# Performance work log

Measured on AMD Instinct MI355X. Metric: run time of the kernel, lower is better.

Reference implementation:

```python
import jax, jax.numpy as jnp
import numpy as np

B, E = 256, 512
C, K = 8192, 10          # n_class, n_center
LMD = 10.0
INV_GAMMA = 10.0         # 1 / gamma, gamma = 0.1
TAU = 0.2
MARGIN = 0.01


def setup_inputs() -> dict:
    key = jax.random.key(0)
    k1, k2, k3 = jax.random.split(key, 3)
    embeddings = jax.random.normal(k1, (B, E), dtype=jnp.float32)
    labels = jax.random.randint(k2, (B,), 0, C, dtype=jnp.int64)
    fc = jax.random.normal(k3, (C * K, E), dtype=jnp.float32)
    return {"embeddings": embeddings, "labels": labels, "fc": fc}


def reference(embeddings, labels, fc):
    # L2-normalize centers (rows of fc), like F.normalize(fc, p=2, dim=1)
    norm = jnp.sqrt(jnp.sum(fc * fc, axis=1, keepdims=True))
    w = fc / jnp.maximum(norm, 1e-12)

    # similarity to every center: [B, C, K]
    x = (embeddings @ w.T).reshape(B, C, K)
    prob = jax.nn.softmax(INV_GAMMA * x, axis=2)
    h = jnp.sum(prob * x, axis=2)  # [B, C] soft-pooled class similarity

    # subtract margin on ground-truth class, then cross-entropy
    rows = jnp.arange(B)
    margin_m = jnp.zeros_like(h).at[rows, labels].set(MARGIN)
    logits = LMD * (h - margin_m)
    logp = jax.nn.log_softmax(logits, axis=1)
    loss_cls = -jnp.mean(logp[rows, labels])

    # regularizer: batched per-class center gram, replaces python loop over C
    wc = w.reshape(C, K, E)
    sub = 1.0 - jnp.einsum('cke,cje->ckj', wc, wc)   # [C, K, K]
    sub = jnp.where(sub <= 0.0, 1e-10, sub)
    mask = jnp.triu(jnp.ones((K, K), dtype=bool), k=1)  # strict upper triangle
    safe = jnp.where(mask, 2.0 * sub, 1.0)
    reg = jnp.sum(jnp.where(mask, jnp.sqrt(safe), 0.0))
    reg = reg / (C * K * (K - 1.0))
    return loss_cls + TAU * reg
```

## Files before the change

### kernel.cpp

```cpp
#include <hip/hip_runtime.h>


typedef __bf16 bf16;
typedef bf16 bf16x8 __attribute__((ext_vector_type(8)));
typedef float f32x4 __attribute__((ext_vector_type(4)));

#define NCLASS 8192
#define KC 10
#define EDIM 512
#define BATCH 256

__device__ inline void load_lds16(const void* g, void* l) {
    __builtin_amdgcn_global_load_lds(
        (const __attribute__((address_space(1))) void*)g,
        (__attribute__((address_space(3))) void*)l, 16, 0, 0);
}

__global__ __launch_bounds__(256) void prep_kernel(
    const float* __restrict__ fc, bf16* __restrict__ w,
    float* __restrict__ gram_part)
{
    __shared__ float rows[KC * EDIM];
    __shared__ float s_invn[KC];
    __shared__ float s_wsum[4];
    const int c = blockIdx.x;
    const int t = threadIdx.x;
    const int wave = t >> 6, lane = t & 63;

    const float4* src = (const float4*)(fc + (size_t)c * (KC * EDIM));
    float4* rows4 = (float4*)rows;
    #pragma unroll
    for (int i = 0; i < 5; ++i) rows4[t + i * 256] = src[t + i * 256];
    __syncthreads();

    for (int r = wave; r < KC; r += 4) {
        float s = 0.f;
        #pragma unroll
        for (int j = 0; j < 8; ++j) {
            float v = rows[r * EDIM + lane + j * 64];
            s += v * v;
        }
        #pragma unroll
        for (int off = 32; off; off >>= 1) s += __shfl_xor(s, off);
        if (lane == 0) s_invn[r] = 1.0f / fmaxf(sqrtf(s), 1e-12f);
    }
    __syncthreads();

    bf16x8* dst = (bf16x8*)(w + (size_t)c * (KC * EDIM));
    #pragma unroll
    for (int p = 0; p < 3; ++p) {
        int j = t + p * 256;
        if (j < 640) {
            int r = j >> 6;
            float inv = s_invn[r];
            float4 a = *(const float4*)(rows + j * 8);
            float4 b = *(const float4*)(rows + j * 8 + 4);
            bf16x8 v;
            v[0] = (bf16)(a.x * inv); v[1] = (bf16)(a.y * inv);
            v[2] = (bf16)(a.z * inv); v[3] = (bf16)(a.w * inv);
            v[4] = (bf16)(b.x * inv); v[5] = (bf16)(b.y * inv);
            v[6] = (bf16)(b.z * inv); v[7] = (bf16)(b.w * inv);
            dst[j] = v;
        }
    }

    float part = 0.f;
    for (int p = wave; p < 45; p += 4) {
        int i = 0, pp = p;
        while (pp >= 9 - i) { pp -= 9 - i; ++i; }
        int j = i + 1 + pp;
        float s = 0.f;
        #pragma unroll
        for (int u = 0; u < 8; ++u)
            s += rows[i * EDIM + lane + u * 64] * rows[j * EDIM + lane + u * 64];
        #pragma unroll
        for (int off = 32; off; off >>= 1) s += __shfl_xor(s, off);
        if (lane == 0) {
            float sub = 1.0f - s * s_invn[i] * s_invn[j];
            if (sub <= 0.0f) sub = 1e-10f;
            part += sqrtf(2.0f * sub);
        }
    }
    if (lane == 0) s_wsum[wave] = part;
    __syncthreads();
    if (t == 0) gram_part[c] = s_wsum[0] + s_wsum[1] + s_wsum[2] + s_wsum[3];
}

__global__ __launch_bounds__(256) void conv_kernel(
    const float* __restrict__ e, bf16* __restrict__ out)
{
    int i = blockIdx.x * 256 + threadIdx.x;
    float4 a = ((const float4*)e)[i * 2];
    float4 b = ((const float4*)e)[i * 2 + 1];
    bf16x8 v;
    v[0] = (bf16)a.x; v[1] = (bf16)a.y; v[2] = (bf16)a.z; v[3] = (bf16)a.w;
    v[4] = (bf16)b.x; v[5] = (bf16)b.y; v[6] = (bf16)b.z; v[7] = (bf16)b.w;
    ((bf16x8*)out)[i] = v;
}

__global__ __launch_bounds__(512) void gemm_h_kernel(
    const bf16* __restrict__ W,
    const bf16* __restrict__ A,
    float* __restrict__ h)
{
    __shared__ bf16 Ws[80 * 32];
    __shared__ bf16 Es[256 * 32];
    const int tid = threadIdx.x;
    const int wave = tid >> 6, lane = tid & 63;

    f32x4 acc[5][2];
    #pragma unroll
    for (int mt = 0; mt < 5; ++mt)
        #pragma unroll
        for (int nt = 0; nt < 2; ++nt)
            acc[mt][nt] = (f32x4){0.f, 0.f, 0.f, 0.f};

    const size_t g0 = (size_t)blockIdx.x * 80;
    const int srow = lane >> 2;
    const int scol = (lane & 3) * 8;

    for (int kb = 0; kb < EDIM; kb += 32) {
        if (wave < 5)
            load_lds16(W + (g0 + (wave << 4) + srow) * EDIM + kb + scol,
                       Ws + ((wave << 4) * 32));
        #pragma unroll
        for (int p = 0; p < 2; ++p) {
            int row = p * 128 + wave * 16 + srow;
            load_lds16(A + row * EDIM + kb + scol,
                       Es + (p * 128 + wave * 16) * 32);
        }
        __syncthreads();

        const int q8 = (lane >> 4) * 8;
        const int fr = lane & 15;
        bf16x8 wf[5], ef[2];
        #pragma unroll
        for (int mt = 0; mt < 5; ++mt)
            wf[mt] = *(const bf16x8*)&Ws[(mt * 16 + fr) * 32 + q8];
        #pragma unroll
        for (int nt = 0; nt < 2; ++nt)
            ef[nt] = *(const bf16x8*)&Es[(wave * 32 + nt * 16 + fr) * 32 + q8];
        #pragma unroll
        for (int mt = 0; mt < 5; ++mt)
            #pragma unroll
            for (int nt = 0; nt < 2; ++nt)
                acc[mt][nt] = __builtin_amdgcn_mfma_f32_16x16x32_bf16(
                    wf[mt], ef[nt], acc[mt][nt], 0, 0, 0);
        __syncthreads();
    }

    const int col = lane & 15;
    const int quad = lane >> 4;
    const int cb = blockIdx.x * 8;
    #pragma unroll
    for (int nt = 0; nt < 2; ++nt) {
        int b = wave * 32 + nt * 16 + col;
        float hval[8];
        #pragma unroll
        for (int c = 0; c < 8; ++c) {
            float xm = -1e30f;
            #pragma unroll
            for (int mt = 0; mt < 5; ++mt) {
                if (10 * c + 10 > 16 * mt && 10 * c < 16 * mt + 16) {
                    #pragma unroll
                    for (int rg = 0; rg < 4; ++rg) {
                        int r = 16 * mt + 4 * quad + rg;
                        if (r >= 10 * c && r < 10 * c + 10)
                            xm = fmaxf(xm, acc[mt][nt][rg]);
                    }
                }
            }
            xm = fmaxf(xm, __shfl_xor(xm, 16));
            xm = fmaxf(xm, __shfl_xor(xm, 32));
            float s1 = 0.f, s2 = 0.f;
            #pragma unroll
            for (int mt = 0; mt < 5; ++mt) {
                if (10 * c + 10 > 16 * mt && 10 * c < 16 * mt + 16) {
                    #pragma unroll
                    for (int rg = 0; rg < 4; ++rg) {
                        int r = 16 * mt + 4 * quad + rg;
                        if (r >= 10 * c && r < 10 * c + 10) {
                            float x = acc[mt][nt][rg];
                            float e = __expf(10.0f * (x - xm));
                            s1 += e; s2 += e * x;
                        }
                    }
                }
            }
            s1 += __shfl_xor(s1, 16); s1 += __shfl_xor(s1, 32);
            s2 += __shfl_xor(s2, 16); s2 += __shfl_xor(s2, 32);
            hval[c] = s2 / s1;
        }
        if (quad == 0) {
            float4 v0 = {hval[0], hval[1], hval[2], hval[3]};
            float4 v1 = {hval[4], hval[5], hval[6], hval[7]};
            float4* dst = (float4*)&h[(size_t)b * NCLASS + cb];
            dst[0] = v0;
            dst[1] = v1;
        }
    }
}

__global__ __launch_bounds__(256) void ce_kernel(
    const float* __restrict__ h, const int* __restrict__ labels,
    float* __restrict__ ce_part)
{
    __shared__ float redm[4];
    __shared__ float reds[4];
    const int b = blockIdx.x, t = threadIdx.x;
    const int wave = t >> 6, lane = t & 63;
    const int lbl = labels[b];
    const float* hb = h + (size_t)b * NCLASS;

    float lg_cache[32];
    float mx = -1e30f;
    #pragma unroll
    for (int k = 0; k < 32; ++k) {
        int c = t + k * 256;
        float lg = 10.0f * hb[c];
        if (c == lbl) lg -= 0.1f;
        lg_cache[k] = lg;
        mx = fmaxf(mx, lg);
    }
    #pragma unroll
    for (int off = 32; off; off >>= 1) mx = fmaxf(mx, __shfl_xor(mx, off));
    if (lane == 0) redm[wave] = mx;
    __syncthreads();
    mx = fmaxf(fmaxf(redm[0], redm[1]), fmaxf(redm[2], redm[3]));

    float s = 0.f;
    #pragma unroll
    for (int k = 0; k < 32; ++k) s += __expf(lg_cache[k] - mx);
    #pragma unroll
    for (int off = 32; off; off >>= 1) s += __shfl_xor(s, off);
    if (lane == 0) reds[wave] = s;
    __syncthreads();
    if (t == 0) {
        s = reds[0] + reds[1] + reds[2] + reds[3];
        float logit_l = 10.0f * (hb[lbl] - 0.01f);
        ce_part[b] = mx + logf(s) - logit_l;
    }
}

__global__ __launch_bounds__(256) void final_kernel(
    const float* __restrict__ gram_part, const float* __restrict__ ce_part,
    float* __restrict__ out)
{
    __shared__ float red[4];
    const int t = threadIdx.x, wave = t >> 6, lane = t & 63;
    float g = 0.f;
    #pragma unroll
    for (int i = 0; i < 32; ++i) g += gram_part[t + i * 256];
    float val = ce_part[t] * (1.0f / 256.0f)
              + g * (0.2f / 737280.0f);
    #pragma unroll
    for (int off = 32; off; off >>= 1) val += __shfl_xor(val, off);
    if (lane == 0) red[wave] = val;
    __syncthreads();
    if (t == 0) out[0] = red[0] + red[1] + red[2] + red[3];
}

extern "C" void kernel_launch(void* const* d_in, const int* in_sizes, int n_in,
                              void* d_out, int out_size, void* d_ws, size_t ws_size,
                              hipStream_t stream) {
    const float* emb    = (const float*)d_in[0];
    const int*   labels = (const int*)d_in[1];
    const float* fc     = (const float*)d_in[2];
    float* out = (float*)d_out;

    char* ws = (char*)d_ws;
    bf16*  w         = (bf16*)ws;
    bf16*  embb      = (bf16*)(ws + 83886080);
    float* h         = (float*)(ws + 84148352);
    float* gram_part = (float*)(ws + 92536960);
    float* ce_part   = (float*)(ws + 92569728);

    prep_kernel<<<NCLASS, 256, 0, stream>>>(fc, w, gram_part);
    conv_kernel<<<64, 256, 0, stream>>>(emb, embb);
    gemm_h_kernel<<<81920 / 80, 512, 0, stream>>>(w, embb, h);
    ce_kernel<<<BATCH, 256, 0, stream>>>(h, labels, ce_part);
    final_kernel<<<1, 256, 0, stream>>>(gram_part, ce_part, out);
}
```

Measured before the change: 306.2 us.

## Fuse center normalization and gram regularizer into the GEMM kernel

Removes the separate prep kernel that wrote normalized bf16 centers to global memory. Each GEMM block now loads its 80 fp32 center rows straight into registers (one wave per class), computes row norms and the pairwise gram regularizer there, and writes the normalized bf16 rows into an XOR-swizzled LDS buffer holding the full K dimension. This drops the 80MB bf16 round trip to global memory and one kernel launch. In exchange each block needs about 96KB of LDS and holds many registers, which may limit occupancy, and the embedding tiles are still streamed per k-step.

```diff
diff --git a/kernel.cpp b/kernel.cpp
--- a/kernel.cpp
+++ b/kernel.cpp
@@ -14,76 +14,6 @@
     __builtin_amdgcn_global_load_lds(
         (const __attribute__((address_space(1))) void*)g,
         (__attribute__((address_space(3))) void*)l, 16, 0, 0);
-}
-
-__global__ __launch_bounds__(256) void prep_kernel(
-    const float* __restrict__ fc, bf16* __restrict__ w,
-    float* __restrict__ gram_part)
-{
-    __shared__ float rows[KC * EDIM];
-    __shared__ float s_invn[KC];
-    __shared__ float s_wsum[4];
-    const int c = blockIdx.x;
-    const int t = threadIdx.x;
-    const int wave = t >> 6, lane = t & 63;
-
-    const float4* src = (const float4*)(fc + (size_t)c * (KC * EDIM));
-    float4* rows4 = (float4*)rows;
-    #pragma unroll
-    for (int i = 0; i < 5; ++i) rows4[t + i * 256] = src[t + i * 256];
-    __syncthreads();
-
-    for (int r = wave; r < KC; r += 4) {
-        float s = 0.f;
-        #pragma unroll
-        for (int j = 0; j < 8; ++j) {
-            float v = rows[r * EDIM + lane + j * 64];
-            s += v * v;
-        }
-        #pragma unroll
-        for (int off = 32; off; off >>= 1) s += __shfl_xor(s, off);
-        if (lane == 0) s_invn[r] = 1.0f / fmaxf(sqrtf(s), 1e-12f);
-    }
-    __syncthreads();
-
-    bf16x8* dst = (bf16x8*)(w + (size_t)c * (KC * EDIM));
-    #pragma unroll
-    for (int p = 0; p < 3; ++p) {
-        int j = t + p * 256;
-        if (j < 640) {
-            int r = j >> 6;
-            float inv = s_invn[r];
-            float4 a = *(const float4*)(rows + j * 8);
-            float4 b = *(const float4*)(rows + j * 8 + 4);
-            bf16x8 v;
-            v[0] = (bf16)(a.x * inv); v[1] = (bf16)(a.y * inv);
-            v[2] = (bf16)(a.z * inv); v[3] = (bf16)(a.w * inv);
-            v[4] = (bf16)(b.x * inv); v[5] = (bf16)(b.y * inv);
-            v[6] = (bf16)(b.z * inv); v[7] = (bf16)(b.w * inv);
-            dst[j] = v;
-        }
-    }
-
-    float part = 0.f;
-    for (int p = wave; p < 45; p += 4) {
-        int i = 0, pp = p;
-        while (pp >= 9 - i) { pp -= 9 - i; ++i; }
-        int j = i + 1 + pp;
-        float s = 0.f;
-        #pragma unroll
-        for (int u = 0; u < 8; ++u)
-            s += rows[i * EDIM + lane + u * 64] * rows[j * EDIM + lane + u * 64];
-        #pragma unroll
-        for (int off = 32; off; off >>= 1) s += __shfl_xor(s, off);
-        if (lane == 0) {
-            float sub = 1.0f - s * s_invn[i] * s_invn[j];
-            if (sub <= 0.0f) sub = 1e-10f;
-            part += sqrtf(2.0f * sub);
-        }
-    }
-    if (lane == 0) s_wsum[wave] = part;
-    __syncthreads();
-    if (t == 0) gram_part[c] = s_wsum[0] + s_wsum[1] + s_wsum[2] + s_wsum[3];
 }
 
 __global__ __launch_bounds__(256) void conv_kernel(
@@ -98,16 +28,67 @@
     ((bf16x8*)out)[i] = v;
 }
 
-__global__ __launch_bounds__(512) void gemm_h_kernel(
-    const bf16* __restrict__ W,
+__global__ __launch_bounds__(512, 2) void fused_kernel(
+    const float* __restrict__ fc,
     const bf16* __restrict__ A,
-    float* __restrict__ h)
-{
-    __shared__ bf16 Ws[80 * 32];
+    float* __restrict__ h,
+    float* __restrict__ gram_part)
+{
+    __shared__ bf16 Wl[80 * EDIM];
     __shared__ bf16 Es[256 * 32];
     const int tid = threadIdx.x;
     const int wave = tid >> 6, lane = tid & 63;
 
+    const int c = blockIdx.x * 8 + wave;
+    float4 ra[KC][2];
+    #pragma unroll
+    for (int r = 0; r < KC; ++r) {
+        const float4* rp =
+            (const float4*)(fc + ((size_t)c * KC + r) * EDIM) + lane * 2;
+        ra[r][0] = rp[0];
+        ra[r][1] = rp[1];
+    }
+    float invn[KC];
+    #pragma unroll
+    for (int r = 0; r < KC; ++r) {
+        float4 a = ra[r][0], b = ra[r][1];
+        float s = a.x*a.x + a.y*a.y + a.z*a.z + a.w*a.w
+                + b.x*b.x + b.y*b.y + b.z*b.z + b.w*b.w;
+        #pragma unroll
+        for (int off = 32; off; off >>= 1) s += __shfl_xor(s, off);
+        invn[r] = 1.0f / fmaxf(sqrtf(s), 1e-12f);
+    }
+    float part = 0.f;
+    #pragma unroll
+    for (int i = 0; i < KC - 1; ++i) {
+        #pragma unroll
+        for (int j = i + 1; j < KC; ++j) {
+            float4 ai = ra[i][0], bi = ra[i][1];
+            float4 aj = ra[j][0], bj = ra[j][1];
+            float s = ai.x*aj.x + ai.y*aj.y + ai.z*aj.z + ai.w*aj.w
+                    + bi.x*bj.x + bi.y*bj.y + bi.z*bj.z + bi.w*bj.w;
+            #pragma unroll
+            for (int off = 32; off; off >>= 1) s += __shfl_xor(s, off);
+            float sub = 1.0f - s * invn[i] * invn[j];
+            if (sub <= 0.0f) sub = 1e-10f;
+            part += sqrtf(2.0f * sub);
+        }
+    }
+    if (lane == 0) gram_part[c] = part;
+
+    #pragma unroll
+    for (int r = 0; r < KC; ++r) {
+        int row = wave * KC + r;
+        float inv = invn[r];
+        float4 a = ra[r][0], b = ra[r][1];
+        bf16x8 v;
+        v[0] = (bf16)(a.x * inv); v[1] = (bf16)(a.y * inv);
+        v[2] = (bf16)(a.z * inv); v[3] = (bf16)(a.w * inv);
+        v[4] = (bf16)(b.x * inv); v[5] = (bf16)(b.y * inv);
+        v[6] = (bf16)(b.z * inv); v[7] = (bf16)(b.w * inv);
+        *(bf16x8*)&Wl[row * EDIM + ((lane ^ (row & 7)) << 3)] = v;
+    }
+
     f32x4 acc[5][2];
     #pragma unroll
     for (int mt = 0; mt < 5; ++mt)
@@ -115,14 +96,10 @@
         for (int nt = 0; nt < 2; ++nt)
             acc[mt][nt] = (f32x4){0.f, 0.f, 0.f, 0.f};
 
-    const size_t g0 = (size_t)blockIdx.x * 80;
     const int srow = lane >> 2;
     const int scol = (lane & 3) * 8;
 
     for (int kb = 0; kb < EDIM; kb += 32) {
-        if (wave < 5)
-            load_lds16(W + (g0 + (wave << 4) + srow) * EDIM + kb + scol,
-                       Ws + ((wave << 4) * 32));
         #pragma unroll
         for (int p = 0; p < 2; ++p) {
             int row = p * 128 + wave * 16 + srow;
@@ -135,8 +112,11 @@
         const int fr = lane & 15;
         bf16x8 wf[5], ef[2];
         #pragma unroll
-        for (int mt = 0; mt < 5; ++mt)
-            wf[mt] = *(const bf16x8*)&Ws[(mt * 16 + fr) * 32 + q8];
+        for (int mt = 0; mt < 5; ++mt) {
+            int row = mt * 16 + fr;
+            wf[mt] = *(const bf16x8*)
+                &Wl[row * EDIM + ((kb + q8) ^ ((row & 7) << 3))];
+        }
         #pragma unroll
         for (int nt = 0; nt < 2; ++nt)
             ef[nt] = *(const bf16x8*)&Es[(wave * 32 + nt * 16 + fr) * 32 + q8];
@@ -157,15 +137,15 @@
         int b = wave * 32 + nt * 16 + col;
         float hval[8];
         #pragma unroll
-        for (int c = 0; c < 8; ++c) {
+        for (int cc = 0; cc < 8; ++cc) {
             float xm = -1e30f;
             #pragma unroll
             for (int mt = 0; mt < 5; ++mt) {
-                if (10 * c + 10 > 16 * mt && 10 * c < 16 * mt + 16) {
+                if (10 * cc + 10 > 16 * mt && 10 * cc < 16 * mt + 16) {
                     #pragma unroll
                     for (int rg = 0; rg < 4; ++rg) {
                         int r = 16 * mt + 4 * quad + rg;
-                        if (r >= 10 * c && r < 10 * c + 10)
+                        if (r >= 10 * cc && r < 10 * cc + 10)
                             xm = fmaxf(xm, acc[mt][nt][rg]);
                     }
                 }
@@ -175,11 +155,11 @@
             float s1 = 0.f, s2 = 0.f;
             #pragma unroll
             for (int mt = 0; mt < 5; ++mt) {
-                if (10 * c + 10 > 16 * mt && 10 * c < 16 * mt + 16) {
+                if (10 * cc + 10 > 16 * mt && 10 * cc < 16 * mt + 16) {
                     #pragma unroll
                     for (int rg = 0; rg < 4; ++rg) {
                         int r = 16 * mt + 4 * quad + rg;
-                        if (r >= 10 * c && r < 10 * c + 10) {
+                        if (r >= 10 * cc && r < 10 * cc + 10) {
                             float x = acc[mt][nt][rg];
                             float e = __expf(10.0f * (x - xm));
                             s1 += e; s2 += e * x;
@@ -189,7 +169,7 @@
             }
             s1 += __shfl_xor(s1, 16); s1 += __shfl_xor(s1, 32);
             s2 += __shfl_xor(s2, 16); s2 += __shfl_xor(s2, 32);
-            hval[c] = s2 / s1;
+            hval[cc] = s2 / s1;
         }
         if (quad == 0) {
             float4 v0 = {hval[0], hval[1], hval[2], hval[3]};
@@ -269,15 +249,13 @@
     float* out = (float*)d_out;
 
     char* ws = (char*)d_ws;
-    bf16*  w         = (bf16*)ws;
-    bf16*  embb      = (bf16*)(ws + 83886080);
-    float* h         = (float*)(ws + 84148352);
-    float* gram_part = (float*)(ws + 92536960);
-    float* ce_part   = (float*)(ws + 92569728);
-
-    prep_kernel<<<NCLASS, 256, 0, stream>>>(fc, w, gram_part);
+    bf16*  embb      = (bf16*)ws;
+    float* h         = (float*)(ws + 262144);
+    float* gram_part = (float*)(ws + 8650752);
+    float* ce_part   = (float*)(ws + 8683520);
+
     conv_kernel<<<64, 256, 0, stream>>>(emb, embb);
-    gemm_h_kernel<<<81920 / 80, 512, 0, stream>>>(w, embb, h);
+    fused_kernel<<<NCLASS / 8, 512, 0, stream>>>(fc, embb, h, gram_part);
     ce_kernel<<<BATCH, 256, 0, stream>>>(h, labels, ce_part);
     final_kernel<<<1, 256, 0, stream>>>(gram_part, ce_part, out);
 }
```

Measured after the change: 323.0 us. 5.5% more time.

## Read embedding fragments directly from global in k-blocked layout, swizzle W LDS tile

Applied to the files above, without the earlier changes.

The embedding conversion kernel now writes bf16 data in a k-blocked layout (32-column slabs), so each wave can read its MFMA B fragments straight from global/L2 instead of staging the whole 256x32 embedding tile through shared memory. The W tile is loaded by 320 threads with an XOR swizzle on the column slot to reduce LDS bank conflicts, and launch bounds request 2 blocks per CU. This cuts LDS traffic and footprint per block, at the cost of uncoalesced-style per-lane global reads of the small, heavily reused embedding matrix.

```diff
diff --git a/kernel.cpp b/kernel.cpp
--- a/kernel.cpp
+++ b/kernel.cpp
@@ -87,24 +87,25 @@
 }
 
 __global__ __launch_bounds__(256) void conv_kernel(
-    const float* __restrict__ e, bf16* __restrict__ out)
+    const float* __restrict__ e, bf16* __restrict__ At)
 {
     int i = blockIdx.x * 256 + threadIdx.x;
+    int row = i >> 6, chunk = i & 63;
+    int k = chunk * 8;
     float4 a = ((const float4*)e)[i * 2];
     float4 b = ((const float4*)e)[i * 2 + 1];
     bf16x8 v;
     v[0] = (bf16)a.x; v[1] = (bf16)a.y; v[2] = (bf16)a.z; v[3] = (bf16)a.w;
     v[4] = (bf16)b.x; v[5] = (bf16)b.y; v[6] = (bf16)b.z; v[7] = (bf16)b.w;
-    ((bf16x8*)out)[i] = v;
-}
-
-__global__ __launch_bounds__(512) void gemm_h_kernel(
+    *(bf16x8*)&At[((k >> 5) << 13) + (row << 5) + (k & 31)] = v;
+}
+
+__global__ __launch_bounds__(512, 2) void gemm_h_kernel(
     const bf16* __restrict__ W,
-    const bf16* __restrict__ A,
+    const bf16* __restrict__ At,
     float* __restrict__ h)
 {
     __shared__ bf16 Ws[80 * 32];
-    __shared__ bf16 Es[256 * 32];
     const int tid = threadIdx.x;
     const int wave = tid >> 6, lane = tid & 63;
 
@@ -116,30 +117,33 @@
             acc[mt][nt] = (f32x4){0.f, 0.f, 0.f, 0.f};
 
     const size_t g0 = (size_t)blockIdx.x * 80;
-    const int srow = lane >> 2;
-    const int scol = (lane & 3) * 8;
+
+    const int srow = tid >> 2;
+    const int gc = (tid & 3) ^ ((srow >> 1) & 3);
+    const bf16* wsrc = W + (g0 + srow) * EDIM + gc * 8;
+
+    const int q = lane >> 4;
+    const int q8 = q * 8;
+    const int fr = lane & 15;
 
     for (int kb = 0; kb < EDIM; kb += 32) {
-        if (wave < 5)
-            load_lds16(W + (g0 + (wave << 4) + srow) * EDIM + kb + scol,
-                       Ws + ((wave << 4) * 32));
-        #pragma unroll
-        for (int p = 0; p < 2; ++p) {
-            int row = p * 128 + wave * 16 + srow;
-            load_lds16(A + row * EDIM + kb + scol,
-                       Es + (p * 128 + wave * 16) * 32);
-        }
+        if (tid < 320)
+            load_lds16(wsrc + kb, Ws + wave * 64 * 8);
         __syncthreads();
 
-        const int q8 = (lane >> 4) * 8;
-        const int fr = lane & 15;
         bf16x8 wf[5], ef[2];
         #pragma unroll
-        for (int mt = 0; mt < 5; ++mt)
-            wf[mt] = *(const bf16x8*)&Ws[(mt * 16 + fr) * 32 + q8];
-        #pragma unroll
-        for (int nt = 0; nt < 2; ++nt)
-            ef[nt] = *(const bf16x8*)&Es[(wave * 32 + nt * 16 + fr) * 32 + q8];
+        for (int nt = 0; nt < 2; ++nt) {
+            int row = wave * 32 + nt * 16 + fr;
+            ef[nt] = *(const bf16x8*)
+                &At[((kb >> 5) << 13) + (row << 5) + q8];
+        }
+        #pragma unroll
+        for (int mt = 0; mt < 5; ++mt) {
+            int row = mt * 16 + fr;
+            int slot = q ^ ((row >> 1) & 3);
+            wf[mt] = *(const bf16x8*)&Ws[row * 32 + slot * 8];
+        }
         #pragma unroll
         for (int mt = 0; mt < 5; ++mt)
             #pragma unroll
@@ -157,15 +161,15 @@
         int b = wave * 32 + nt * 16 + col;
         float hval[8];
         #pragma unroll
-        for (int c = 0; c < 8; ++c) {
+        for (int cc = 0; cc < 8; ++cc) {
             float xm = -1e30f;
             #pragma unroll
             for (int mt = 0; mt < 5; ++mt) {
-                if (10 * c + 10 > 16 * mt && 10 * c < 16 * mt + 16) {
+                if (10 * cc + 10 > 16 * mt && 10 * cc < 16 * mt + 16) {
                     #pragma unroll
                     for (int rg = 0; rg < 4; ++rg) {
                         int r = 16 * mt + 4 * quad + rg;
-                        if (r >= 10 * c && r < 10 * c + 10)
+                        if (r >= 10 * cc && r < 10 * cc + 10)
                             xm = fmaxf(xm, acc[mt][nt][rg]);
                     }
                 }
@@ -175,11 +179,11 @@
             float s1 = 0.f, s2 = 0.f;
             #pragma unroll
             for (int mt = 0; mt < 5; ++mt) {
-                if (10 * c + 10 > 16 * mt && 10 * c < 16 * mt + 16) {
+                if (10 * cc + 10 > 16 * mt && 10 * cc < 16 * mt + 16) {
                     #pragma unroll
                     for (int rg = 0; rg < 4; ++rg) {
                         int r = 16 * mt + 4 * quad + rg;
-                        if (r >= 10 * c && r < 10 * c + 10) {
+                        if (r >= 10 * cc && r < 10 * cc + 10) {
                             float x = acc[mt][nt][rg];
                             float e = __expf(10.0f * (x - xm));
                             s1 += e; s2 += e * x;
@@ -189,7 +193,7 @@
             }
             s1 += __shfl_xor(s1, 16); s1 += __shfl_xor(s1, 32);
             s2 += __shfl_xor(s2, 16); s2 += __shfl_xor(s2, 32);
-            hval[c] = s2 / s1;
+            hval[cc] = s2 / s1;
         }
         if (quad == 0) {
             float4 v0 = {hval[0], hval[1], hval[2], hval[3]};
@@ -270,14 +274,14 @@
 
     char* ws = (char*)d_ws;
     bf16*  w         = (bf16*)ws;
-    bf16*  embb      = (bf16*)(ws + 83886080);
+    bf16*  At        = (bf16*)(ws + 83886080);
     float* h         = (float*)(ws + 84148352);
     float* gram_part = (float*)(ws + 92536960);
     float* ce_part   = (float*)(ws + 92569728);
 
     prep_kernel<<<NCLASS, 256, 0, stream>>>(fc, w, gram_part);
-    conv_kernel<<<64, 256, 0, stream>>>(emb, embb);
-    gemm_h_kernel<<<81920 / 80, 512, 0, stream>>>(w, embb, h);
+    conv_kernel<<<64, 256, 0, stream>>>(emb, At);
+    gemm_h_kernel<<<81920 / 80, 512, 0, stream>>>(w, At, h);
     ce_kernel<<<BATCH, 256, 0, stream>>>(h, labels, ce_part);
     final_kernel<<<1, 256, 0, stream>>>(gram_part, ce_part, out);
 }
```

After: 302.3 us. No clear change (-1.3%).
